# Performance work log

Measured on AMD Instinct MI355X. Metric: run time of the kernel, lower is better.

The kernel has to match this reference:

```python
import jax, jax.numpy as jnp
import numpy as np
import math

# ---- module hyperparameters (from init_kwargs) ----
N = 3            # polynomial points per segment
SEGMENTS = 512   # piecewise segments over [-1, 1] (length = 2.0)
ROTATIONS = 4    # -> 2*ROTATIONS stripe directions
WIDTH = 512
HEIGHT = 512
MAX_DIM = max(WIDTH, HEIGHT)
RATIO = MAX_DIM / (MAX_DIM + 1)
NUM_POS = 2 * ROTATIONS
NW = SEGMENTS * (N - 1) + 1  # continuous piecewise weights per channel

# Chebyshev-Lobatto interpolation points on [-1, 1]
CHEB = (-np.cos(np.pi * np.arange(N) / (N - 1))).astype(np.float32)


def make_positions():
    """Rotated stripe position maps, [2*ROTATIONS, WIDTH, HEIGHT], precomputed buffers."""
    xv, yv = np.meshgrid(np.arange(WIDTH), np.arange(HEIGHT), indexing='ij')
    xv = xv.astype(np.float32)
    yv = yv.astype(np.float32)
    pos = []
    for i in range(ROTATIONS):
        theta = math.pi / 2.0 * (i / ROTATIONS)
        cx, cy = math.cos(theta), math.sin(theta)
        for sgn in (1.0, -1.0):  # r1 = cx*x + cy*y, r2 = cx*x - cy*y
            r = cx * xv + sgn * cy * yv
            rmin, rmax = r.min(), r.max()
            dr = rmax - rmin
            r = ((r - rmin) * RATIO / dr - 0.5) * MAX_DIM
            pos.append(r)
    return np.stack(pos, 0).astype(np.float32)


POSITIONS = jnp.asarray(make_positions())  # [8, W, H] constant buffer


def lagrange_basis(t):
    """Lagrange basis at Chebyshev-Lobatto points; t [...], returns [..., N]."""
    bs = []
    for k in range(N):
        b = jnp.ones_like(t)
        for j in range(N):
            if j != k:
                b = b * (t - CHEB[j]) / (CHEB[k] - CHEB[j])
        bs.append(b)
    return jnp.stack(bs, axis=-1)


def piecewise_shared(xin, w):
    """Continuous piecewise Lagrange polynomial, weights shared across positions.
    xin: [B, C, L] in ~[-1, 1]; w: [C, NW]. Returns [B, C, L]."""
    xs = (xin + 1.0) * (0.5 * SEGMENTS)              # segment-space coordinate
    sid = jnp.clip(jnp.floor(xs), 0.0, SEGMENTS - 1)  # segment index (clamped)
    t = 2.0 * (xs - sid) - 1.0                        # local coord in [-1, 1]
    sid = sid.astype(jnp.int32)
    widx = sid[..., None] * (N - 1) + jnp.arange(N)   # [B, C, L, N] weight gather idx
    cidx = jnp.arange(w.shape[0])[None, :, None, None]
    wg = w[cidx, widx]                                # [B, C, L, N]
    return jnp.sum(lagrange_basis(t) * wg, axis=-1)


def setup_inputs() -> dict:
    key = jax.random.key(0)
    k1, k2 = jax.random.split(key)
    x = jax.random.normal(k1, (16, 3, WIDTH, HEIGHT), dtype=jnp.float32)
    weights = jax.random.normal(k2, (NUM_POS, 3, NW), dtype=jnp.float32)  # weight_magnitude=1
    return {"x": x, "weights": weights}


def reference(x, weights):
    B, C, W, H = x.shape
    accum = jnp.zeros((B, C, W * H), dtype=x.dtype)
    for i in range(NUM_POS):
        # position_encode: pixel value perturbs its stripe position, then rescale to [-1,1]
        dl = (0.5 * x + POSITIONS[i]) / (0.5 * MAX_DIM)  # [B, C, W, H]
        dl = dl.reshape(B, C, W * H)
        accum = accum + piecewise_shared(dl, weights[i])
    accum = accum / NUM_POS
    return accum.reshape(x.shape)
```

## Files before the change

kernel.cpp:

```cpp
#include <hip/hip_runtime.h>
#include <math.h>


#define WDIM 512
#define HDIM 512
#define SEGS 512
#define NPOS 8
#define NTAB 7
#define NW   1025
#define CCH  3

#define THREADS 512
#define TILE 64
#define TILES_PER_SLICE ((WDIM / TILE) * (HDIM / TILE))

struct Params {
    float ax[NPOS];
    float ay[NPOS];
    float c0[NPOS];
};

union HalfPack {
    unsigned int u;
    _Float16 h[2];
};

__global__ __launch_bounds__(THREADS, 8)
void stripe_poly_kernel(const float* __restrict__ x,
                        const float* __restrict__ w,
                        float* __restrict__ out,
                        Params P)
{
    __shared__ uint2 lut[NTAB][SEGS];

    const int slice = blockIdx.x / TILES_PER_SLICE;
    const int tile  = blockIdx.x % TILES_PER_SLICE;
    const int ch    = slice % CCH;
    const int bx    = (tile >> 3) * TILE;
    const int by    = (tile & 7) * TILE;

    for (int idx = threadIdx.x; idx < NTAB * SEGS; idx += THREADS) {
        const int m = idx >> 9;
        const int s = idx & (SEGS - 1);
        float w0, w1, w2;
        if (m == 0) {
            const float* wa = w + (size_t)(0 * CCH + ch) * NW + 2 * s;
            const float* wb = w + (size_t)(1 * CCH + ch) * NW + 2 * s;
            w0 = wa[0] + wb[0]; w1 = wa[1] + wb[1]; w2 = wa[2] + wb[2];
        } else {
            const float* wp = w + (size_t)((m + 1) * CCH + ch) * NW + 2 * s;
            w0 = wp[0]; w1 = wp[1]; w2 = wp[2];
        }
        const float c0 = 0.125f * w1;
        const float c1 = 0.0625f * (w2 - w0);
        const float c2 = 0.125f * fmaf(0.5f, w0 + w2, -w1);
        HalfPack hp;
        hp.h[0] = (_Float16)c1;
        hp.h[1] = (_Float16)c2;
        lut[m][s] = make_uint2(__float_as_uint(c0), hp.u);
    }
    __syncthreads();

    const int tid  = threadIdx.x;
    const int wv   = tid >> 6;
    const int lane = tid & 63;
    const int px_w = (wv >> 2) * 16;
    const int py_w = (wv & 3) * 16;
    const int px_l = lane >> 2;
    const int py_l = (lane & 3) * 4;

    const size_t slice_off = (size_t)slice * (WDIM * HDIM);
    const int py = by + py_w + py_l;
    const float yf = (float)py;

    for (int k = 0; k < 2; ++k) {
        const int px = bx + px_w + k * 32 + px_l;
        const size_t p0 = slice_off + (size_t)px * HDIM + py;
        const float4 xin = *(const float4*)(x + p0);
        const float xf = (float)px;
        const float xv[4] = {xin.x, xin.y, xin.z, xin.w};
        float acc[4] = {0.f, 0.f, 0.f, 0.f};

        #pragma unroll
        for (int i = 0; i < NTAB; ++i) {
            const int pi = (i == 0) ? 0 : (i + 1);
            const float ay = P.ay[pi];
            const float g  = fmaf(ay, yf, fmaf(P.ax[pi], xf, P.c0[pi]));
            #pragma unroll
            for (int j = 0; j < 4; ++j) {
                const float xs = fmaf(0.5f, xv[j], fmaf(ay, (float)j, g));
                float sf = floorf(xs);
                sf = fminf(fmaxf(sf, 0.0f), (float)(SEGS - 1));
                const int s = (int)sf;
                const float t = fmaf(2.0f, xs - sf, -1.0f);
                const uint2 v = lut[i][s];
                HalfPack hp; hp.u = v.y;
                const float u = fmaf(t, (float)hp.h[1], (float)hp.h[0]);
                acc[j] = fmaf(t, u, acc[j] + __uint_as_float(v.x));
            }
        }

        float4 o;
        o.x = acc[0]; o.y = acc[1]; o.z = acc[2]; o.w = acc[3];
        *(float4*)(out + p0) = o;
    }
}

extern "C" void kernel_launch(void* const* d_in, const int* in_sizes, int n_in,
                              void* d_out, int out_size, void* d_ws, size_t ws_size,
                              hipStream_t stream)
{
    const float* x = (const float*)d_in[0];
    const float* w = (const float*)d_in[1];
    float* out = (float*)d_out;

    Params P;
    const double ratio_f = (double)(float)(512.0 / 513.0);
    for (int i = 0; i < 4; ++i) {
        const double theta = (M_PI * 0.5) * ((double)i / 4.0);
        const float a   = (float)cos(theta);
        const float cyf = (float)sin(theta);
        for (int sg = 0; sg < 2; ++sg) {
            const float b = (sg == 0) ? cyf : -cyf;
            const float ax511 = a * 511.0f;
            const float by511 = b * 511.0f;
            float rmin, rmax;
            if (sg == 0) { rmin = 0.0f;  rmax = ax511 + by511; }
            else         { rmin = by511; rmax = ax511; }
            const float dr = rmax - rmin;
            const double K = 512.0 * ratio_f / (double)dr;
            const int pi = 2 * i + sg;
            P.ax[pi] = (float)(K * (double)a);
            P.ay[pi] = (float)(K * (double)b);
            P.c0[pi] = (float)(-K * (double)rmin);
        }
    }

    const int slices = in_sizes[0] / (WDIM * HDIM);
    const int blocks = slices * TILES_PER_SLICE;
    stripe_poly_kernel<<<blocks, THREADS, 0, stream>>>(x, w, out, P);
}
```

Before: 117.3 us.

## Enlarge pixel tile per block, prefetch next input row, hoist position math

Each block now covers a 128x64 pixel tile with four row iterations instead of a 64x64 tile with two. This halves the number of blocks that rebuild the 7x512 shared-memory coefficient table from global weights, so the table build is spread over twice as many pixels. The next float4 of input is loaded before the current one is computed, to overlap memory latency. The y-dependent part of the stripe coordinate is hoisted out of the loop, and the per-column offsets are formed by repeated addition. The tradeoff is fewer blocks, which lowers parallelism, and slightly different rounding of the coordinate near segment boundaries.

```diff
diff --git a/kernel.cpp b/kernel.cpp
--- a/kernel.cpp
+++ b/kernel.cpp
@@ -11,8 +11,10 @@
 #define CCH  3
 
 #define THREADS 512
-#define TILE 64
-#define TILES_PER_SLICE ((WDIM / TILE) * (HDIM / TILE))
+#define TILE_X 128
+#define TILE_Y 64
+#define KITER  4
+#define TILES_PER_SLICE ((WDIM / TILE_X) * (HDIM / TILE_Y))
 
 struct Params {
     float ax[NPOS];
@@ -36,8 +38,8 @@
     const int slice = blockIdx.x / TILES_PER_SLICE;
     const int tile  = blockIdx.x % TILES_PER_SLICE;
     const int ch    = slice % CCH;
-    const int bx    = (tile >> 3) * TILE;
-    const int by    = (tile & 7) * TILE;
+    const int bx    = (tile >> 3) * TILE_X;
+    const int by    = (tile & 7) * TILE_Y;
 
     for (int idx = threadIdx.x; idx < NTAB * SEGS; idx += THREADS) {
         const int m = idx >> 9;
@@ -64,20 +66,29 @@
     const int tid  = threadIdx.x;
     const int wv   = tid >> 6;
     const int lane = tid & 63;
-    const int px_w = (wv >> 2) * 16;
-    const int py_w = (wv & 3) * 16;
-    const int px_l = lane >> 2;
-    const int py_l = (lane & 3) * 4;
+    const int px0  = bx + (wv >> 2) * 16 + (lane >> 2);
+    const int py   = by + (wv & 3) * 16 + (lane & 3) * 4;
+    const float yf = (float)py;
 
     const size_t slice_off = (size_t)slice * (WDIM * HDIM);
-    const int py = by + py_w + py_l;
-    const float yf = (float)py;
+    const size_t pbase = slice_off + (size_t)px0 * HDIM + py;
 
-    for (int k = 0; k < 2; ++k) {
-        const int px = bx + px_w + k * 32 + px_l;
-        const size_t p0 = slice_off + (size_t)px * HDIM + py;
-        const float4 xin = *(const float4*)(x + p0);
-        const float xf = (float)px;
+    float gy[NTAB];
+    #pragma unroll
+    for (int i = 0; i < NTAB; ++i) {
+        const int pi = (i == 0) ? 0 : (i + 1);
+        gy[i] = fmaf(P.ay[pi], yf, P.c0[pi]);
+    }
+
+    float4 xin = *(const float4*)(x + pbase);
+    #pragma unroll
+    for (int k = 0; k < KITER; ++k) {
+        const size_t pk = pbase + (size_t)(k * 32) * HDIM;
+        float4 xnext;
+        if (k + 1 < KITER)
+            xnext = *(const float4*)(x + pk + (size_t)32 * HDIM);
+
+        const float xf = (float)(px0 + k * 32);
         const float xv[4] = {xin.x, xin.y, xin.z, xin.w};
         float acc[4] = {0.f, 0.f, 0.f, 0.f};
 
@@ -85,10 +96,15 @@
         for (int i = 0; i < NTAB; ++i) {
             const int pi = (i == 0) ? 0 : (i + 1);
             const float ay = P.ay[pi];
-            const float g  = fmaf(ay, yf, fmaf(P.ax[pi], xf, P.c0[pi]));
+            const float g  = fmaf(P.ax[pi], xf, gy[i]);
+            float gj[4];
+            gj[0] = g;
+            gj[1] = g + ay;
+            gj[2] = gj[1] + ay;
+            gj[3] = gj[2] + ay;
             #pragma unroll
             for (int j = 0; j < 4; ++j) {
-                const float xs = fmaf(0.5f, xv[j], fmaf(ay, (float)j, g));
+                const float xs = fmaf(0.5f, xv[j], gj[j]);
                 float sf = floorf(xs);
                 sf = fminf(fmaxf(sf, 0.0f), (float)(SEGS - 1));
                 const int s = (int)sf;
@@ -102,7 +118,8 @@
 
         float4 o;
         o.x = acc[0]; o.y = acc[1]; o.z = acc[2]; o.w = acc[3];
-        *(float4*)(out + p0) = o;
+        *(float4*)(out + pk) = o;
+        xin = xnext;
     }
 }
 
```

Measured after the change: 114.0 us. 2.8% less time.
